# Kernel optimization log

Measured on AMD Instinct MI355X. Metric: run time of the kernel, lower is better.

## Reference

```python
import jax, jax.numpy as jnp
import numpy as np

SIZE = 64            # size
DIST = 4             # distance (4x4x4 unshared window)
PAD = DIST // 2      # 2
DS = SIZE - 4        # depth of voxel grid (60)
CONVEY = 0.9
RATE = 5
FC_IN = DS * SIZE * SIZE  # (size-4)*size*size = 245760


def setup_inputs() -> dict:
    key = jax.random.key(0)
    ks = jax.random.split(key, 8)
    vinput = jax.random.normal(ks[0], (DS, SIZE, SIZE, 4), dtype=jnp.float32)
    # location-specific (unshared) 4x4x4 synapse weights per voxel
    synapse = jax.random.normal(ks[1], (DS, SIZE, SIZE, DIST, DIST, DIST), dtype=jnp.float32)
    W1 = jax.random.normal(ks[2], (1024, FC_IN), dtype=jnp.float32) / np.float32(np.sqrt(FC_IN))
    b1 = jnp.zeros((1024,), jnp.float32)
    W2 = jax.random.normal(ks[3], (128, 1024), dtype=jnp.float32) / np.float32(np.sqrt(1024))
    b2 = jnp.zeros((128,), jnp.float32)
    W3 = jax.random.normal(ks[4], (10, 128), dtype=jnp.float32) / np.float32(np.sqrt(128))
    b3 = jnp.zeros((10,), jnp.float32)
    return {"vinput": vinput, "synapse": synapse, "W1": W1, "b1": b1,
            "W2": W2, "b2": b2, "W3": W3, "b3": b3}


def _forward(vinput, synapse, W1, b1, W2, b2, W3, b3):
    # frame is zeros, so neuron_matrix = pad(vinput) on the 3 spatial dims
    nm = jnp.pad(vinput, ((PAD, PAD), (PAD, PAD), (PAD, PAD), (0, 0)))  # (DS+2P, S+2P, S+2P, 4)
    ofs = jnp.arange(DIST)
    # gather indices for the 4x4x4 windows anchored at the top-left (as in the source)
    wi = (jnp.arange(DS)[:, None] + ofs)[:, None, None, :, None, None]
    wj = (jnp.arange(SIZE)[:, None] + ofs)[None, :, None, None, :, None]
    wk = (jnp.arange(SIZE)[:, None] + ofs)[None, None, :, None, None, :]
    for _ in range(RATE):
        # synapse (d,d,d) broadcasts over channel, so the full sum factors
        # through the channel-sum of the neuron matrix.
        ns = nm.sum(-1)                       # (DS+2P, S+2P, S+2P)
        win = ns[wi, wj, wk]                  # (DS, S, S, d, d, d)
        core = jnp.einsum('ijkabc,ijkabc->ijk', synapse, win)  # (DS, S, S)
        # dummy is written only at [0:DS, 0:S, 0:S]; border stays zero.
        nm = jnp.zeros_like(nm).at[:DS, :SIZE, :SIZE, :].set(
            (jax.nn.relu(core) * CONVEY)[..., None])
    x = nm[PAD:DS + PAD, PAD:SIZE + PAD, PAD:SIZE + PAD, :]  # (DS, S, S, 4)
    x = x.reshape(-1, FC_IN)                                 # (4, FC_IN), row-major like torch view
    x = jax.nn.relu(x @ W1.T + b1)
    x = jax.nn.relu(x @ W2.T + b2)
    return x @ W3.T + b3                                     # (4, 10)


def reference(vinput, synapse, W1, b1, W2, b2, W3, b3):
    return _forward(vinput, synapse, W1, b1, W2, b2, W3, b3)
```

## Files before the change

kernel.cpp:

```cpp
#include <hip/hip_runtime.h>

#define DSX 60
#define SZ  64
#define NPT (DSX*SZ*SZ)
#define NS_P 64
#define NS_Q 68
#define NS_R 68
#define NS_SZ (NS_P*NS_Q*NS_R)
#define P_PER_ROW 61440
#define KSPLIT 8
#define P_CHUNK (P_PER_ROW / KSPLIT)
#define PB_SLAB (15*NS_Q*NS_R)
#define NS_BLOCKS 1156
#define TR_BLOCKS (NPT / 64)

typedef float fx4 __attribute__((ext_vector_type(4)));

__device__ __forceinline__ unsigned rne_bf16(float x) {
    unsigned b = __float_as_uint(x);
    return (b + 0x7fffu + ((b >> 16) & 1u)) >> 16;
}

__global__ __launch_bounds__(256) void prologue(const float* __restrict__ vin,
                                                const float* __restrict__ syn,
                                                float* __restrict__ PB0,
                                                float* __restrict__ PB1,
                                                uint2* __restrict__ synP) {
    if (blockIdx.x < NS_BLOCKS) {
        int t = blockIdx.x * 256 + threadIdx.x;
        if (t >= NS_SZ) return;
        int r = t % NS_R;
        int q = (t / NS_R) % NS_Q;
        int p = t / (NS_R * NS_Q);
        float val = 0.f;
        if (p >= 2 && p < 62 && q >= 2 && q < 66 && r >= 2 && r < 66) {
            const float* b = vin + ((((size_t)(p - 2) * SZ) + (q - 2)) * SZ + (r - 2)) * 4;
            val = (b[0] + b[1]) + (b[2] + b[3]);
        }
        PB0[t] = val;
        PB1[t] = 0.f;
    } else {
        __shared__ float tile[64 * 65];
        int t0 = (blockIdx.x - NS_BLOCKS) * 64;
        const fx4* s4 = (const fx4*)syn;
#pragma unroll
        for (int r = 0; r < 4; r++) {
            int idx = r * 256 + threadIdx.x;
            int pl = idx >> 4, g = idx & 15;
            fx4 v = s4[(size_t)(t0 + pl) * 16 + g];
            int base = pl * 65 + g * 4;
            tile[base] = v.x; tile[base + 1] = v.y; tile[base + 2] = v.z; tile[base + 3] = v.w;
        }
        __syncthreads();
        int l = threadIdx.x & 63;
        int wv = threadIdx.x >> 6;
#pragma unroll
        for (int r = 0; r < 4; r++) {
            int g = r * 4 + wv;
            int base = l * 65 + g * 4;
            uint2 u;
            u.x = rne_bf16(tile[base])     | (rne_bf16(tile[base + 1]) << 16);
            u.y = rne_bf16(tile[base + 2]) | (rne_bf16(tile[base + 3]) << 16);
            synP[(size_t)g * NPT + t0 + l] = u;
        }
    }
}

__global__ __launch_bounds__(256) void conv_kernel(const float* __restrict__ PBin,
                                                   const uint2* __restrict__ synP,
                                                   float* __restrict__ PBout) {
    int t = blockIdx.x * 256 + threadIdx.x;
    int k = t & 63;
    int j = (t >> 6) & 63;
    int i = t >> 12;
    float acc = 0.f;
#pragma unroll
    for (int g = 0; g < 16; g++) {
        uint2 u = synP[(size_t)g * NPT + t];
        float w0 = __uint_as_float(u.x << 16);
        float w1 = __uint_as_float(u.x & 0xffff0000u);
        float w2 = __uint_as_float(u.y << 16);
        float w3 = __uint_as_float(u.y & 0xffff0000u);
        int a = g >> 2, b = g & 3;
        const float* nrow = PBin + ((size_t)(i + a) * NS_Q + (j + b)) * NS_R + k;
        acc += w0 * nrow[0] + w1 * nrow[1] + w2 * nrow[2] + w3 * nrow[3];
    }
    PBout[((size_t)i * NS_Q + j) * NS_R + k] = acc > 0.f ? acc * 3.6f : 0.f;
}

__global__ __launch_bounds__(256) void gemv1(const float* __restrict__ W1,
                                             const float* __restrict__ PB,
                                             float* __restrict__ partial) {
    int n = blockIdx.x >> 3;
    int c = blockIdx.x & 7;
    const fx4* w4 = (const fx4*)(W1 + (size_t)n * (P_PER_ROW * 4));
    float a0 = 0.f, a1 = 0.f, a2 = 0.f, a3 = 0.f;
#pragma unroll 5
    for (int it = 0; it < P_CHUNK / 256; it++) {
        int p = c * P_CHUNK + it * 256 + threadIdx.x;
        fx4 w = __builtin_nontemporal_load(&w4[p]);
        float s = (w.x + w.y) + (w.z + w.w);
        int iloc = p >> 12;
        int j = (p >> 6) & 63;
        int k = p & 63;
        int base = ((iloc + 2) * NS_Q + (j + 2)) * NS_R + (k + 2);
        a0 += s * PB[base];
        a1 += s * PB[base + PB_SLAB];
        a2 += s * PB[base + 2 * PB_SLAB];
        a3 += s * PB[base + 3 * PB_SLAB];
    }
#pragma unroll
    for (int off = 32; off; off >>= 1) {
        a0 += __shfl_down(a0, off);
        a1 += __shfl_down(a1, off);
        a2 += __shfl_down(a2, off);
        a3 += __shfl_down(a3, off);
    }
    __shared__ float red[4][4];
    int lane = threadIdx.x & 63, wv = threadIdx.x >> 6;
    if (lane == 0) { red[wv][0] = a0; red[wv][1] = a1; red[wv][2] = a2; red[wv][3] = a3; }
    __syncthreads();
    if (threadIdx.x < 4) {
        int r = threadIdx.x;
        float s = (red[0][r] + red[1][r]) + (red[2][r] + red[3][r]);
        partial[((size_t)c * 4 + r) * 1024 + n] = s;
    }
}

__global__ __launch_bounds__(256) void fc2(const float* __restrict__ W2,
                                           const float* __restrict__ b1,
                                           const float* __restrict__ b2,
                                           const float* __restrict__ partial,
                                           float* __restrict__ h2) {
    int n = blockIdx.x;
    float a0 = 0.f, a1 = 0.f, a2 = 0.f, a3 = 0.f;
    for (int e = threadIdx.x; e < 1024; e += 256) {
        float w = W2[(size_t)n * 1024 + e];
        float be = b1[e];
#pragma unroll
        for (int r = 0; r < 4; r++) {
            float acc = 0.f;
#pragma unroll
            for (int cc = 0; cc < KSPLIT; cc++) acc += partial[(cc * 4 + r) * 1024 + e];
            float h = 0.25f * acc + be;
            h = h > 0.f ? h : 0.f;
            if (r == 0) a0 += w * h;
            else if (r == 1) a1 += w * h;
            else if (r == 2) a2 += w * h;
            else a3 += w * h;
        }
    }
#pragma unroll
    for (int off = 32; off; off >>= 1) {
        a0 += __shfl_down(a0, off);
        a1 += __shfl_down(a1, off);
        a2 += __shfl_down(a2, off);
        a3 += __shfl_down(a3, off);
    }
    __shared__ float red[4][4];
    int lane = threadIdx.x & 63, wv = threadIdx.x >> 6;
    if (lane == 0) { red[wv][0] = a0; red[wv][1] = a1; red[wv][2] = a2; red[wv][3] = a3; }
    __syncthreads();
    if (threadIdx.x < 4) {
        int r = threadIdx.x;
        float s = (red[0][r] + red[1][r]) + (red[2][r] + red[3][r]) + b2[n];
        h2[(size_t)r * 128 + n] = s > 0.f ? s : 0.f;
    }
}

__global__ __launch_bounds__(64) void fc3(const float* __restrict__ W3,
                                          const float* __restrict__ b3,
                                          const float* __restrict__ h2,
                                          float* __restrict__ out) {
    int t = threadIdx.x;
    if (t < 40) {
        int r = t / 10, n = t % 10;
        float a = b3[n];
        for (int e = 0; e < 128; e++) a += W3[(size_t)n * 128 + e] * h2[(size_t)r * 128 + e];
        out[t] = a;
    }
}

extern "C" void kernel_launch(void* const* d_in, const int* in_sizes, int n_in,
                              void* d_out, int out_size, void* d_ws, size_t ws_size,
                              hipStream_t stream) {
    const float* vin = (const float*)d_in[0];
    const float* syn = (const float*)d_in[1];
    const float* W1  = (const float*)d_in[2];
    const float* b1  = (const float*)d_in[3];
    const float* W2  = (const float*)d_in[4];
    const float* b2  = (const float*)d_in[5];
    const float* W3  = (const float*)d_in[6];
    const float* b3  = (const float*)d_in[7];
    float* out = (float*)d_out;

    float* ws = (float*)d_ws;
    float* PB0 = ws;
    float* PB1 = PB0 + NS_SZ;
    float* partial = PB1 + NS_SZ;
    float* h2 = partial + 32 * 1024;
    uint2* synP = (uint2*)(h2 + 1024);

    const int ptBlocks = NPT / 256;

    prologue<<<NS_BLOCKS + TR_BLOCKS, 256, 0, stream>>>(vin, syn, PB0, PB1, synP);
    float* cur = PB0; float* nxt = PB1;
    for (int it = 0; it < 5; it++) {
        conv_kernel<<<ptBlocks, 256, 0, stream>>>(cur, synP, nxt);
        float* tmp = cur; cur = nxt; nxt = tmp;
    }
    gemv1<<<1024 * KSPLIT, 256, 0, stream>>>(W1, cur, partial);
    fc2<<<128, 256, 0, stream>>>(W2, b1, b2, partial, h2);
    fc3<<<1, 64, 0, stream>>>(W3, b3, h2, out);
}
```

Baseline: 253.5 us.

## Prefetch W1 slices into cache during conv launches and drop nontemporal loads

Each of the five conv launches gets 512 extra blocks that stream a separate 32 MB slice of W1. They reduce it to a value that is never really used, so the bytes end up resident in the large last-level cache before gemv1 runs. gemv1 now uses normal loads instead of nontemporal ones, so it can hit those cached lines, and it processes two W1 vectors per iteration to raise memory-level parallelism. The aim is to hide part of the 1 GB W1 stream behind the conv stages. The extra traffic lengthens each conv launch, and later W1 reads may evict the prefetched data if the cache cannot hold it.

```diff
diff --git a/kernel.cpp b/kernel.cpp
--- a/kernel.cpp
+++ b/kernel.cpp
@@ -13,6 +13,9 @@
 #define PB_SLAB (15*NS_Q*NS_R)
 #define NS_BLOCKS 1156
 #define TR_BLOCKS (NPT / 64)
+#define PT_BLOCKS (NPT / 256)
+#define PF_BLOCKS 512
+#define PF_ITERS  16
 
 typedef float fx4 __attribute__((ext_vector_type(4)));
 
@@ -68,24 +71,41 @@
 
 __global__ __launch_bounds__(256) void conv_kernel(const float* __restrict__ PBin,
                                                    const uint2* __restrict__ synP,
-                                                   float* __restrict__ PBout) {
-    int t = blockIdx.x * 256 + threadIdx.x;
-    int k = t & 63;
-    int j = (t >> 6) & 63;
-    int i = t >> 12;
-    float acc = 0.f;
-#pragma unroll
-    for (int g = 0; g < 16; g++) {
-        uint2 u = synP[(size_t)g * NPT + t];
-        float w0 = __uint_as_float(u.x << 16);
-        float w1 = __uint_as_float(u.x & 0xffff0000u);
-        float w2 = __uint_as_float(u.y << 16);
-        float w3 = __uint_as_float(u.y & 0xffff0000u);
-        int a = g >> 2, b = g & 3;
-        const float* nrow = PBin + ((size_t)(i + a) * NS_Q + (j + b)) * NS_R + k;
-        acc += w0 * nrow[0] + w1 * nrow[1] + w2 * nrow[2] + w3 * nrow[3];
-    }
-    PBout[((size_t)i * NS_Q + j) * NS_R + k] = acc > 0.f ? acc * 3.6f : 0.f;
+                                                   float* __restrict__ PBout,
+                                                   const float* __restrict__ W1,
+                                                   float* __restrict__ pfdump,
+                                                   int slice) {
+    if (blockIdx.x < PT_BLOCKS) {
+        int t = blockIdx.x * 256 + threadIdx.x;
+        int k = t & 63;
+        int j = (t >> 6) & 63;
+        int i = t >> 12;
+        float acc = 0.f;
+#pragma unroll
+        for (int g = 0; g < 16; g++) {
+            uint2 u = synP[(size_t)g * NPT + t];
+            float w0 = __uint_as_float(u.x << 16);
+            float w1 = __uint_as_float(u.x & 0xffff0000u);
+            float w2 = __uint_as_float(u.y << 16);
+            float w3 = __uint_as_float(u.y & 0xffff0000u);
+            int a = g >> 2, b = g & 3;
+            const float* nrow = PBin + ((size_t)(i + a) * NS_Q + (j + b)) * NS_R + k;
+            acc += w0 * nrow[0] + w1 * nrow[1] + w2 * nrow[2] + w3 * nrow[3];
+        }
+        PBout[((size_t)i * NS_Q + j) * NS_R + k] = acc > 0.f ? acc * 3.6f : 0.f;
+    } else {
+        int b = blockIdx.x - PT_BLOCKS;
+        const fx4* w = (const fx4*)W1 +
+            (size_t)slice * (PF_BLOCKS * 256 * PF_ITERS) +
+            (size_t)b * (256 * PF_ITERS) + threadIdx.x;
+        float acc = 0.f;
+#pragma unroll
+        for (int it = 0; it < PF_ITERS; it++) {
+            fx4 v = w[it * 256];
+            acc += (v.x + v.y) + (v.z + v.w);
+        }
+        if (acc == 1234.56789f) pfdump[b] = acc;
+    }
 }
 
 __global__ __launch_bounds__(256) void gemv1(const float* __restrict__ W1,
@@ -96,18 +116,21 @@
     const fx4* w4 = (const fx4*)(W1 + (size_t)n * (P_PER_ROW * 4));
     float a0 = 0.f, a1 = 0.f, a2 = 0.f, a3 = 0.f;
 #pragma unroll 5
-    for (int it = 0; it < P_CHUNK / 256; it++) {
-        int p = c * P_CHUNK + it * 256 + threadIdx.x;
-        fx4 w = __builtin_nontemporal_load(&w4[p]);
-        float s = (w.x + w.y) + (w.z + w.w);
-        int iloc = p >> 12;
-        int j = (p >> 6) & 63;
-        int k = p & 63;
-        int base = ((iloc + 2) * NS_Q + (j + 2)) * NS_R + (k + 2);
-        a0 += s * PB[base];
-        a1 += s * PB[base + PB_SLAB];
-        a2 += s * PB[base + 2 * PB_SLAB];
-        a3 += s * PB[base + 3 * PB_SLAB];
+    for (int it = 0; it < 15; it++) {
+        int p1 = c * P_CHUNK + it * 256 + threadIdx.x;
+        int p2 = p1 + 15 * 256;
+        fx4 wa = w4[p1];
+        fx4 wb = w4[p2];
+        float sa = (wa.x + wa.y) + (wa.z + wa.w);
+        float sb = (wb.x + wb.y) + (wb.z + wb.w);
+        int i1 = p1 >> 12, j1 = (p1 >> 6) & 63, k1 = p1 & 63;
+        int i2 = p2 >> 12, j2 = (p2 >> 6) & 63, k2 = p2 & 63;
+        int base1 = ((i1 + 2) * NS_Q + (j1 + 2)) * NS_R + (k1 + 2);
+        int base2 = ((i2 + 2) * NS_Q + (j2 + 2)) * NS_R + (k2 + 2);
+        a0 += sa * PB[base1] + sb * PB[base2];
+        a1 += sa * PB[base1 + PB_SLAB] + sb * PB[base2 + PB_SLAB];
+        a2 += sa * PB[base1 + 2 * PB_SLAB] + sb * PB[base2 + 2 * PB_SLAB];
+        a3 += sa * PB[base1 + 3 * PB_SLAB] + sb * PB[base2 + 3 * PB_SLAB];
     }
 #pragma unroll
     for (int off = 32; off; off >>= 1) {
@@ -199,14 +222,13 @@
     float* PB1 = PB0 + NS_SZ;
     float* partial = PB1 + NS_SZ;
     float* h2 = partial + 32 * 1024;
-    uint2* synP = (uint2*)(h2 + 1024);
-
-    const int ptBlocks = NPT / 256;
+    float* pfdump = h2 + 1024;
+    uint2* synP = (uint2*)(pfdump + 1024);
 
     prologue<<<NS_BLOCKS + TR_BLOCKS, 256, 0, stream>>>(vin, syn, PB0, PB1, synP);
     float* cur = PB0; float* nxt = PB1;
     for (int it = 0; it < 5; it++) {
-        conv_kernel<<<ptBlocks, 256, 0, stream>>>(cur, synP, nxt);
+        conv_kernel<<<PT_BLOCKS + PF_BLOCKS, 256, 0, stream>>>(cur, synP, nxt, W1, pfdump, it);
         float* tmp = cur; cur = nxt; nxt = tmp;
     }
     gemv1<<<1024 * KSPLIT, 256, 0, stream>>>(W1, cur, partial);
```

After: 263.2 us. +3.9%, slower.

## Pre-reduce W1 to bf16 channel sums overlapped with prologue and conv passes

Applied to the files above, without the earlier changes.

The channel-sum reduction of W1, which gemv1 previously did while streaming about 1 GB of fp32 weights, is now split into six slices. Each slice runs as extra blocks inside the prologue or one of the five conv launches, and writes packed bf16 sums to a workspace buffer. gemv1 then reads the much smaller bf16 buffer with KSPLIT reduced to 4. The aim is to hide the dominant W1 read bandwidth behind the latency-bound conv iterations. The cost is an extra write and read of the reduced weights, plus bf16 rounding of the summed weights.

```diff
diff --git a/kernel.cpp b/kernel.cpp
--- a/kernel.cpp
+++ b/kernel.cpp
@@ -8,11 +8,16 @@
 #define NS_R 68
 #define NS_SZ (NS_P*NS_Q*NS_R)
 #define P_PER_ROW 61440
-#define KSPLIT 8
-#define P_CHUNK (P_PER_ROW / KSPLIT)
+#define KSPLIT 4
 #define PB_SLAB (15*NS_Q*NS_R)
 #define NS_BLOCKS 1156
 #define TR_BLOCKS (NPT / 64)
+#define PT_BLOCKS (NPT / 256)
+#define RD_BLOCKS 1024
+#define TOT_PAIRS 31457280
+#define SLICE_PAIRS (TOT_PAIRS / 6)
+#define BLOCK_PAIRS (SLICE_PAIRS / RD_BLOCKS)
+#define THREAD_PAIRS (BLOCK_PAIRS / 256)
 
 typedef float fx4 __attribute__((ext_vector_type(4)));
 
@@ -21,13 +26,33 @@
     return (b + 0x7fffu + ((b >> 16) & 1u)) >> 16;
 }
 
+__device__ __forceinline__ void reduce_w1_slice(const float* __restrict__ W1,
+                                                unsigned* __restrict__ W1r,
+                                                int slice, int b) {
+    const fx4* w4 = (const fx4*)W1;
+    size_t base = (size_t)slice * SLICE_PAIRS + (size_t)b * BLOCK_PAIRS + threadIdx.x;
+#pragma unroll
+    for (int it = 0; it < THREAD_PAIRS; it++) {
+        size_t P = base + (size_t)it * 256;
+        fx4 a = __builtin_nontemporal_load(&w4[2 * P]);
+        fx4 c = __builtin_nontemporal_load(&w4[2 * P + 1]);
+        float s0 = (a.x + a.y) + (a.z + a.w);
+        float s1 = (c.x + c.y) + (c.z + c.w);
+        W1r[P] = rne_bf16(s0) | (rne_bf16(s1) << 16);
+    }
+}
+
 __global__ __launch_bounds__(256) void prologue(const float* __restrict__ vin,
                                                 const float* __restrict__ syn,
+                                                const float* __restrict__ W1,
                                                 float* __restrict__ PB0,
                                                 float* __restrict__ PB1,
-                                                uint2* __restrict__ synP) {
-    if (blockIdx.x < NS_BLOCKS) {
-        int t = blockIdx.x * 256 + threadIdx.x;
+                                                uint2* __restrict__ synP,
+                                                unsigned* __restrict__ W1r) {
+    if (blockIdx.x < RD_BLOCKS) {
+        reduce_w1_slice(W1, W1r, 0, blockIdx.x);
+    } else if (blockIdx.x < RD_BLOCKS + NS_BLOCKS) {
+        int t = (blockIdx.x - RD_BLOCKS) * 256 + threadIdx.x;
         if (t >= NS_SZ) return;
         int r = t % NS_R;
         int q = (t / NS_R) % NS_Q;
@@ -41,7 +66,7 @@
         PB1[t] = 0.f;
     } else {
         __shared__ float tile[64 * 65];
-        int t0 = (blockIdx.x - NS_BLOCKS) * 64;
+        int t0 = (blockIdx.x - RD_BLOCKS - NS_BLOCKS) * 64;
         const fx4* s4 = (const fx4*)syn;
 #pragma unroll
         for (int r = 0; r < 4; r++) {
@@ -68,46 +93,61 @@
 
 __global__ __launch_bounds__(256) void conv_kernel(const float* __restrict__ PBin,
                                                    const uint2* __restrict__ synP,
-                                                   float* __restrict__ PBout) {
-    int t = blockIdx.x * 256 + threadIdx.x;
-    int k = t & 63;
-    int j = (t >> 6) & 63;
-    int i = t >> 12;
-    float acc = 0.f;
-#pragma unroll
-    for (int g = 0; g < 16; g++) {
-        uint2 u = synP[(size_t)g * NPT + t];
-        float w0 = __uint_as_float(u.x << 16);
-        float w1 = __uint_as_float(u.x & 0xffff0000u);
-        float w2 = __uint_as_float(u.y << 16);
-        float w3 = __uint_as_float(u.y & 0xffff0000u);
-        int a = g >> 2, b = g & 3;
-        const float* nrow = PBin + ((size_t)(i + a) * NS_Q + (j + b)) * NS_R + k;
-        acc += w0 * nrow[0] + w1 * nrow[1] + w2 * nrow[2] + w3 * nrow[3];
-    }
-    PBout[((size_t)i * NS_Q + j) * NS_R + k] = acc > 0.f ? acc * 3.6f : 0.f;
-}
-
-__global__ __launch_bounds__(256) void gemv1(const float* __restrict__ W1,
+                                                   float* __restrict__ PBout,
+                                                   const float* __restrict__ W1,
+                                                   unsigned* __restrict__ W1r,
+                                                   int slice) {
+    if (blockIdx.x < RD_BLOCKS) {
+        reduce_w1_slice(W1, W1r, slice, blockIdx.x);
+    } else {
+        int t = (blockIdx.x - RD_BLOCKS) * 256 + threadIdx.x;
+        int k = t & 63;
+        int j = (t >> 6) & 63;
+        int i = t >> 12;
+        float acc = 0.f;
+#pragma unroll
+        for (int g = 0; g < 16; g++) {
+            uint2 u = synP[(size_t)g * NPT + t];
+            float w0 = __uint_as_float(u.x << 16);
+            float w1 = __uint_as_float(u.x & 0xffff0000u);
+            float w2 = __uint_as_float(u.y << 16);
+            float w3 = __uint_as_float(u.y & 0xffff0000u);
+            int a = g >> 2, b = g & 3;
+            const float* nrow = PBin + ((size_t)(i + a) * NS_Q + (j + b)) * NS_R + k;
+            acc += w0 * nrow[0] + w1 * nrow[1] + w2 * nrow[2] + w3 * nrow[3];
+        }
+        PBout[((size_t)i * NS_Q + j) * NS_R + k] = acc > 0.f ? acc * 3.6f : 0.f;
+    }
+}
+
+__global__ __launch_bounds__(256) void gemv1(const unsigned* __restrict__ W1r,
                                              const float* __restrict__ PB,
                                              float* __restrict__ partial) {
-    int n = blockIdx.x >> 3;
-    int c = blockIdx.x & 7;
-    const fx4* w4 = (const fx4*)(W1 + (size_t)n * (P_PER_ROW * 4));
+    int n = blockIdx.x >> 2;
+    int c = blockIdx.x & 3;
+    const uint2* w2 = (const uint2*)W1r + (size_t)n * 15360 + c * 3840;
     float a0 = 0.f, a1 = 0.f, a2 = 0.f, a3 = 0.f;
 #pragma unroll 5
-    for (int it = 0; it < P_CHUNK / 256; it++) {
-        int p = c * P_CHUNK + it * 256 + threadIdx.x;
-        fx4 w = __builtin_nontemporal_load(&w4[p]);
-        float s = (w.x + w.y) + (w.z + w.w);
-        int iloc = p >> 12;
-        int j = (p >> 6) & 63;
-        int k = p & 63;
-        int base = ((iloc + 2) * NS_Q + (j + 2)) * NS_R + (k + 2);
-        a0 += s * PB[base];
-        a1 += s * PB[base + PB_SLAB];
-        a2 += s * PB[base + 2 * PB_SLAB];
-        a3 += s * PB[base + 3 * PB_SLAB];
+    for (int it = 0; it < 15; it++) {
+        int u = it * 256 + threadIdx.x;
+        uint2 w = w2[u];
+        float w0 = __uint_as_float(w.x << 16);
+        float w1 = __uint_as_float(w.x & 0xffff0000u);
+        float w2f = __uint_as_float(w.y << 16);
+        float w3 = __uint_as_float(w.y & 0xffff0000u);
+        int p0 = c * 15360 + u * 4;
+        int iloc = p0 >> 12;
+        int j = (p0 >> 6) & 63;
+        int k0 = p0 & 63;
+        int base = ((iloc + 2) * NS_Q + (j + 2)) * NS_R + (k0 + 2);
+        const float* pb0 = PB + base;
+        a0 += w0 * pb0[0] + w1 * pb0[1] + w2f * pb0[2] + w3 * pb0[3];
+        const float* pb1 = pb0 + PB_SLAB;
+        a1 += w0 * pb1[0] + w1 * pb1[1] + w2f * pb1[2] + w3 * pb1[3];
+        const float* pb2 = pb0 + 2 * PB_SLAB;
+        a2 += w0 * pb2[0] + w1 * pb2[1] + w2f * pb2[2] + w3 * pb2[3];
+        const float* pb3 = pb0 + 3 * PB_SLAB;
+        a3 += w0 * pb3[0] + w1 * pb3[1] + w2f * pb3[2] + w3 * pb3[3];
     }
 #pragma unroll
     for (int off = 32; off; off >>= 1) {
@@ -198,18 +238,17 @@
     float* PB0 = ws;
     float* PB1 = PB0 + NS_SZ;
     float* partial = PB1 + NS_SZ;
-    float* h2 = partial + 32 * 1024;
+    float* h2 = partial + 16 * 1024;
     uint2* synP = (uint2*)(h2 + 1024);
-
-    const int ptBlocks = NPT / 256;
-
-    prologue<<<NS_BLOCKS + TR_BLOCKS, 256, 0, stream>>>(vin, syn, PB0, PB1, synP);
+    unsigned* W1r = (unsigned*)(synP + (size_t)NPT * 16);
+
+    prologue<<<RD_BLOCKS + NS_BLOCKS + TR_BLOCKS, 256, 0, stream>>>(vin, syn, W1, PB0, PB1, synP, W1r);
     float* cur = PB0; float* nxt = PB1;
     for (int it = 0; it < 5; it++) {
-        conv_kernel<<<ptBlocks, 256, 0, stream>>>(cur, synP, nxt);
+        conv_kernel<<<RD_BLOCKS + PT_BLOCKS, 256, 0, stream>>>(cur, synP, nxt, W1, W1r, it + 1);
         float* tmp = cur; cur = nxt; nxt = tmp;
     }
-    gemv1<<<1024 * KSPLIT, 256, 0, stream>>>(W1, cur, partial);
+    gemv1<<<1024 * KSPLIT, 256, 0, stream>>>(W1r, cur, partial);
     fc2<<<128, 256, 0, stream>>>(W2, b1, b2, partial, h2);
     fc3<<<1, 64, 0, stream>>>(W3, b3, h2, out);
 }
```

After: 327.2 us. +29.1%, slower.
